# Performance work log

Measured on AMD Instinct MI355X. Metric: run time of the kernel, lower is better.

## Reference

```python
import jax, jax.numpy as jnp
import numpy as np
from functools import partial

G, N, E = 512, 256, 1024
F_IN, EMB, H, NCLS = 30, 256, 3, 2
NEG_SLOPE = 0.2
K1 = int(np.ceil(0.8 * N))   # 205
K2 = int(np.ceil(0.8 * K1))  # 164
K3 = int(np.ceil(0.8 * K2))  # 132


def _gat(x, src, dst, emask, W, asrc, adst, b):
    # Single-graph GATConv (PyG semantics, eval mode): x [n,f], edges [e] + validity mask.
    # Adds self-loops (PyG default), edge-softmax grouped by destination node.
    n = x.shape[0]
    h = (x @ W.T).reshape(n, H, EMB)                      # [n,H,C]
    a_s = (h * asrc).sum(-1)                              # [n,H]
    a_d = (h * adst).sum(-1)                              # [n,H]
    loops = jnp.arange(n, dtype=src.dtype)
    s = jnp.concatenate([src, loops])
    d = jnp.concatenate([dst, loops])
    m = jnp.concatenate([emask, jnp.ones((n,), bool)])
    logit = jax.nn.leaky_relu(a_s[s] + a_d[d], NEG_SLOPE)  # [e+n,H]
    logit = jnp.where(m[:, None], logit, -1e9)
    mx = jax.ops.segment_max(logit, d, num_segments=n)     # stable softmax per dst
    w = jnp.exp(logit - mx[d]) * m[:, None]
    den = jax.ops.segment_sum(w, d, num_segments=n)
    alpha = w / den[d]
    out = jax.ops.segment_sum(alpha[:, :, None] * h[s], d, num_segments=n)  # [n,H,C]
    return out.reshape(n, H * EMB) + b


def _pool(x, src, dst, emask, p, k):
    # TopKPooling: score = tanh((x.p)/||p||); keep top-k nodes, scale by score,
    # remap edge indices and invalidate edges touching dropped nodes.
    n = x.shape[0]
    score = jnp.tanh((x @ p) / jnp.linalg.norm(p))
    vals, perm = jax.lax.top_k(score, k)
    xn = x[perm] * vals[:, None]
    inv = jnp.full((n,), -1, jnp.int32).at[perm].set(jnp.arange(k, dtype=jnp.int32))
    ns, nd = inv[src], inv[dst]
    nm = emask & (ns >= 0) & (nd >= 0)
    return xn, jnp.maximum(ns, 0), jnp.maximum(nd, 0), nm


_gat_b = jax.vmap(_gat, in_axes=(0, 0, 0, 0, None, None, None, None))


def _pool_b(x, src, dst, m, p, k):
    return jax.vmap(partial(_pool, k=k), in_axes=(0, 0, 0, 0, None))(x, src, dst, m, p)


def _readout(x):
    # global_max_pool || global_mean_pool per graph: [G,n,d] -> [G,2d]
    return jnp.concatenate([x.max(axis=1), x.mean(axis=1)], axis=-1)


def _forward(x, edge_src, edge_dst, params):
    (W1, as1, ad1, b1, ht1w, ht1b, p1,
     W2, as2, ad2, b2, ht2w, ht2b, p2,
     W3, as3, ad3, b3, ht3w, ht3b, p3,
     l1w, l1b, l2w, l2b) = params
    src, dst = edge_src, edge_dst
    m = jnp.ones(src.shape, bool)
    h = _gat_b(x, src, dst, m, W1, as1, ad1, b1) @ ht1w.T + ht1b
    h, src, dst, m = _pool_b(h, src, dst, m, p1, K1)
    x1 = _readout(h)
    h = _gat_b(h, src, dst, m, W2, as2, ad2, b2) @ ht2w.T + ht2b
    h, src, dst, m = _pool_b(h, src, dst, m, p2, K2)
    x2 = _readout(h)
    h = _gat_b(h, src, dst, m, W3, as3, ad3, b3) @ ht3w.T + ht3b
    h, src, dst, m = _pool_b(h, src, dst, m, p3, K3)
    x3 = _readout(h)
    z = x1 + x2 + x3
    z = jax.nn.relu(z @ l1w.T + l1b)  # F.dropout is a no-op in eval mode
    return z @ l2w.T + l2b


def setup_inputs() -> dict:
    key = jax.random.key(0)
    keys = iter(jax.random.split(key, 64))
    def nrm(shape, s=0.05):
        return jax.random.normal(next(keys), shape, jnp.float32) * s
    inp = {
        "x": jax.random.normal(next(keys), (G, N, F_IN), jnp.float32),
        "edge_src": jax.random.randint(next(keys), (G, E), 0, N, jnp.int32),
        "edge_dst": jax.random.randint(next(keys), (G, E), 0, N, jnp.int32),
    }
    for i, fin in ((1, F_IN), (2, EMB), (3, EMB)):
        inp[f"W{i}"] = nrm((H * EMB, fin))
        inp[f"asrc{i}"] = nrm((H, EMB))
        inp[f"adst{i}"] = nrm((H, EMB))
        inp[f"b{i}"] = jnp.zeros((H * EMB,), jnp.float32)
        inp[f"ht{i}_w"] = nrm((EMB, H * EMB))
        inp[f"ht{i}_b"] = jnp.zeros((EMB,), jnp.float32)
        inp[f"p{i}"] = nrm((EMB,), 1.0)
    inp["lin1_w"] = nrm((EMB, 2 * EMB))
    inp["lin1_b"] = jnp.zeros((EMB,), jnp.float32)
    inp["lin2_w"] = nrm((NCLS, EMB))
    inp["lin2_b"] = jnp.zeros((NCLS,), jnp.float32)
    return inp


def reference(x, edge_src, edge_dst,
              W1, asrc1, adst1, b1, ht1_w, ht1_b, p1,
              W2, asrc2, adst2, b2, ht2_w, ht2_b, p2,
              W3, asrc3, adst3, b3, ht3_w, ht3_b, p3,
              lin1_w, lin1_b, lin2_w, lin2_b):
    params = (W1, asrc1, adst1, b1, ht1_w, ht1_b, p1,
              W2, asrc2, adst2, b2, ht2_w, ht2_b, p2,
              W3, asrc3, adst3, b3, ht3_w, ht3_b, p3,
              lin1_w, lin1_b, lin2_w, lin2_b)
    return _forward(x, edge_src, edge_dst, params)
```

## Files before the change

kernel.cpp:

```cpp
#include <hip/hip_runtime.h>
#include <hip/hip_bf16.h>

#define GG 512
#define NMAX 256
#define EE 1024
#define HH 3
#define EMB 256
#define NEDGE 1280
#define NEG 0.2f

typedef __attribute__((ext_vector_type(8))) short bf16x8;
typedef __attribute__((ext_vector_type(4))) float f32x4;
#define MFMA16(A,B,C) __builtin_amdgcn_mfma_f32_16x16x32_bf16((A),(B),(C),0,0,0)

__device__ inline void bsplit(float v, unsigned short& s0, unsigned short& s1,
                              unsigned short& s2) {
  __hip_bfloat16 b0 = __float2bfloat16(v);
  float r1 = v - __bfloat162float(b0);
  __hip_bfloat16 b1 = __float2bfloat16(r1);
  float r2 = r1 - __bfloat162float(b1);
  __hip_bfloat16 b2 = __float2bfloat16(r2);
  s0 = *(unsigned short*)&b0; s1 = *(unsigned short*)&b1; s2 = *(unsigned short*)&b2;
}

__global__ void k_prep_wa(const float* __restrict__ W, const float* __restrict__ asrc,
                          const float* __restrict__ adst, float* __restrict__ wa_s,
                          float* __restrict__ wa_d, int f) {
  int t = blockIdx.x * blockDim.x + threadIdx.x;
  int tot = HH * f;
  if (t >= 2 * tot) return;
  int which = t / tot;
  int r = t - which * tot;
  int hd = r / f, ff = r - hd * f;
  const float* a = which ? adst : asrc;
  float s = 0.f;
  for (int c = 0; c < EMB; ++c)
    s += a[hd * EMB + c] * W[(size_t)(hd * EMB + c) * f + ff];
  (which ? wa_d : wa_s)[r] = s;
}

__global__ void k_prep_mcatP(const float* __restrict__ W, const float* __restrict__ htw,
                             float* __restrict__ mcat, int f, int KP) {
  int t = blockIdx.x * blockDim.x + threadIdx.x;
  if (t >= KP * EMB) return;
  int row = t >> 8, j = t & 255;
  float s = 0.f;
  if (row < 3 * f) {
    int hd = row / f, ff = row - hd * f;
    for (int c = 0; c < EMB; ++c)
      s += htw[(size_t)j * (HH * EMB) + hd * EMB + c] * W[(size_t)(hd * EMB + c) * f + ff];
  }
  mcat[(size_t)row * EMB + j] = s;
}

__global__ void k_prep_bt3(const float* __restrict__ mcat, unsigned short* __restrict__ B0,
                           unsigned short* __restrict__ B1, unsigned short* __restrict__ B2,
                           int KP) {
  int t = blockIdx.x * blockDim.x + threadIdx.x;
  if (t >= 256 * KP) return;
  int n = t / KP, k = t - n * KP;
  float v = mcat[(size_t)k * 256 + n];
  unsigned short s0, s1, s2;
  bsplit(v, s0, s1, s2);
  B0[t] = s0; B1[t] = s1; B2[t] = s2;
}

__global__ void k_prep_bb(const float* __restrict__ b, const float* __restrict__ htw,
                          const float* __restrict__ htb, float* __restrict__ bb) {
  int j = threadIdx.x;
  float s = htb[j];
  for (int k = 0; k < HH * EMB; ++k) s += b[k] * htw[(size_t)j * (HH * EMB) + k];
  bb[j] = s;
}

__global__ void k_prep_q(const float* __restrict__ mcat, const float* __restrict__ p,
                         double* __restrict__ qv, int f) {
  int r = blockIdx.x * blockDim.x + threadIdx.x;
  if (r >= 3 * f) return;
  double s = 0.0;
  for (int c = 0; c < EMB; ++c) s += (double)mcat[(size_t)r * EMB + c] * (double)p[c];
  qv[r] = s;
}

__global__ void k_prep_sc(const float* __restrict__ p, const float* __restrict__ bb,
                          double* __restrict__ sc2) {
  __shared__ double sh[256], sh2[256];
  int t = threadIdx.x;
  double pv = (double)p[t];
  sh[t] = pv * pv;
  sh2[t] = (double)bb[t] * pv;
  __syncthreads();
  for (int s = 128; s > 0; s >>= 1) {
    if (t < s) { sh[t] += sh[t + s]; sh2[t] += sh2[t + s]; }
    __syncthreads();
  }
  if (t == 0) { sc2[0] = sh2[0]; sc2[1] = sqrt(sh[0]); }
}

__global__ __launch_bounds__(256) void k_graph(
    const int* __restrict__ src_in, const int* __restrict__ dst_in, int first,
    int* __restrict__ es, int* __restrict__ ed, int* __restrict__ em,
    const float* __restrict__ xin, const float* __restrict__ wa_s,
    const float* __restrict__ wa_d, const double* __restrict__ qv,
    const double* __restrict__ sc2,
    float4* __restrict__ a4, int* __restrict__ coff, int* __restrict__ elist,
    int* __restrict__ sel, float* __restrict__ val, int n_in, int f, int kout) {
  __shared__ float lgs[NEDGE * 3];
  __shared__ unsigned short sdst[NEDGE], ssrc[NEDGE];
  __shared__ unsigned char sval[NEDGE];
  __shared__ float sas[256][3], sad[256][3];
  __shared__ double stdt[256][3];
  __shared__ int cnt2[256];
  __shared__ int off[257];
  __shared__ int elist_s[NEDGE];
  __shared__ float sscore[256];
  __shared__ unsigned long long keys[256];
  __shared__ int inv[256];
  int g = blockIdx.x, tid = threadIdx.x;
  int etot = EE + n_in;
  cnt2[tid] = 0;
  if (tid < n_in) {
    const float* xr = xin + ((size_t)g * n_in + tid) * f;
    float s0 = 0, s1 = 0, s2 = 0, d0 = 0, d1 = 0, d2 = 0;
    double t0 = 0, t1 = 0, t2 = 0;
    for (int c = 0; c < f; ++c) {
      float xv = xr[c];
      s0 += xv * wa_s[c]; s1 += xv * wa_s[f + c]; s2 += xv * wa_s[2 * f + c];
      d0 += xv * wa_d[c]; d1 += xv * wa_d[f + c]; d2 += xv * wa_d[2 * f + c];
      double xd = (double)xv;
      t0 += xd * qv[c]; t1 += xd * qv[f + c]; t2 += xd * qv[2 * f + c];
    }
    sas[tid][0] = s0; sas[tid][1] = s1; sas[tid][2] = s2;
    sad[tid][0] = d0; sad[tid][1] = d1; sad[tid][2] = d2;
    stdt[tid][0] = t0; stdt[tid][1] = t1; stdt[tid][2] = t2;
  }
  __syncthreads();
  for (int e = tid; e < etot; e += 256) {
    int s, d, v;
    if (e < EE) {
      if (first) { s = src_in[g * EE + e]; d = dst_in[g * EE + e]; v = 1; }
      else { s = es[g * EE + e]; d = ed[g * EE + e]; v = em[g * EE + e]; }
    } else { s = d = e - EE; v = 1; }
    sdst[e] = (unsigned short)d; ssrc[e] = (unsigned short)s; sval[e] = (unsigned char)v;
    if (v) {
#pragma unroll
      for (int h = 0; h < HH; ++h) {
        float lv = sas[s][h] + sad[d][h];
        lgs[e * 3 + h] = lv > 0.f ? lv : NEG * lv;
      }
      atomicAdd(&cnt2[d], 1);
    }
  }
  __syncthreads();
  if (tid == 0) {
    int run = 0;
    for (int i = 0; i < n_in; ++i) { int c = cnt2[i]; off[i] = run; run += c; }
    off[n_in] = run;
  }
  __syncthreads();
  for (int i = tid; i <= n_in; i += 256) coff[g * 257 + i] = off[i];
  cnt2[tid] = 0;
  __syncthreads();
  for (int e = tid; e < etot; e += 256) {
    if (sval[e]) {
      int d = sdst[e];
      int pos = atomicAdd(&cnt2[d], 1);
      elist_s[off[d] + pos] = e;
    }
  }
  __syncthreads();
  if (tid < n_in) {
    int o0 = off[tid], o1 = off[tid + 1];
    for (int i = o0 + 1; i < o1; ++i) {
      int key = elist_s[i];
      int j = i - 1;
      while (j >= o0 && elist_s[j] > key) { elist_s[j + 1] = elist_s[j]; --j; }
      elist_s[j + 1] = key;
    }
    for (int q = o0; q < o1; ++q) elist[g * NEDGE + q] = elist_s[q];
  }
  __syncthreads();
  float sc = -3e38f;
  if (tid < n_in) {
    int o0 = off[tid], o1 = off[tid + 1];
    float m0 = -1e30f, m1 = -1e30f, m2 = -1e30f;
    for (int q = o0; q < o1; ++q) {
      int e = elist_s[q];
      m0 = fmaxf(m0, lgs[e * 3 + 0]);
      m1 = fmaxf(m1, lgs[e * 3 + 1]);
      m2 = fmaxf(m2, lgs[e * 3 + 2]);
    }
    float d0 = 0, d1 = 0, d2 = 0;
    for (int q = o0; q < o1; ++q) {
      int e = elist_s[q];
      d0 += expf(lgs[e * 3 + 0] - m0);
      d1 += expf(lgs[e * 3 + 1] - m1);
      d2 += expf(lgs[e * 3 + 2] - m2);
    }
    float r0 = 1.f / d0, r1 = 1.f / d1, r2 = 1.f / d2;
    double s = 0.0;
    for (int q = o0; q < o1; ++q) {
      int e = elist_s[q];
      float w0 = expf(lgs[e * 3 + 0] - m0) * r0;
      float w1 = expf(lgs[e * 3 + 1] - m1) * r1;
      float w2 = expf(lgs[e * 3 + 2] - m2) * r2;
      int src = ssrc[e];
      float4 av; av.x = w0; av.y = w1; av.z = w2; av.w = __int_as_float(src);
      a4[(size_t)g * NEDGE + e] = av;
      s += (double)w0 * stdt[src][0] + (double)w1 * stdt[src][1] + (double)w2 * stdt[src][2];
    }
    sc = (float)tanh((s + sc2[0]) / sc2[1]);
  }
  sscore[tid] = sc;
  unsigned int u = __float_as_uint(sc);
  unsigned int ord = (u & 0x80000000u) ? ~u : (u | 0x80000000u);
  unsigned long long key = ((unsigned long long)(~ord) << 32) | (unsigned int)tid;
  if (tid >= n_in) key = 0xFFFFFFFF00000000ull | (unsigned int)tid;
  keys[tid] = key;
  __syncthreads();
  for (int kk = 2; kk <= 256; kk <<= 1) {
    for (int j = kk >> 1; j > 0; j >>= 1) {
      int ixj = tid ^ j;
      if (ixj > tid) {
        unsigned long long a = keys[tid], b = keys[ixj];
        bool up = ((tid & kk) == 0);
        if (up ? (a > b) : (a < b)) { keys[tid] = b; keys[ixj] = a; }
      }
      __syncthreads();
    }
  }
  inv[tid] = -1;
  __syncthreads();
  if (tid < kout) {
    int pi = (int)(keys[tid] & 0xFFFFu);
    inv[pi] = tid;
    sel[g * 256 + tid] = pi;
    val[g * 256 + tid] = sscore[pi];
  }
  __syncthreads();
  for (int e = tid; e < EE; e += 256) {
    int s = ssrc[e], d = sdst[e], m = sval[e];
    int ns = inv[s], nd = inv[d];
    int nm = (m && ns >= 0 && nd >= 0) ? 1 : 0;
    es[g * EE + e] = ns < 0 ? 0 : ns;
    ed[g * EE + e] = nd < 0 ? 0 : nd;
    em[g * EE + e] = nm;
  }
}

template<bool F256>
__global__ __launch_bounds__(256) void k_gather_sel(
    const float* __restrict__ xin, const float4* __restrict__ a4,
    const int* __restrict__ coff, const int* __restrict__ elist,
    const int* __restrict__ sel,
    unsigned short* __restrict__ A0, unsigned short* __restrict__ A1,
    unsigned short* __restrict__ A2,
    int gc, int n_in, int n_out, int f, int KP) {
  int wid = (blockIdx.x * blockDim.x + threadIdx.x) >> 6;
  int lane = threadIdx.x & 63;
  if (wid >= gc * n_out) return;
  int g = wid / n_out, j = wid - g * n_out;
  int pi = sel[(g << 8) + j];
  int o0 = coff[g * 257 + pi], o1 = coff[g * 257 + pi + 1];
  const float* xg = xin + (size_t)g * n_in * f;
  size_t rb = ((size_t)g * n_out + j) * (size_t)KP;
  if (F256) {
    float4 acc0 = make_float4(0, 0, 0, 0);
    float4 acc1 = make_float4(0, 0, 0, 0);
    float4 acc2 = make_float4(0, 0, 0, 0);
    for (int t = o0; t < o1; ++t) {
      int e = elist[g * NEDGE + t];
      float4 a = a4[(size_t)g * NEDGE + e];
      int src = __float_as_int(a.w);
      float4 xv = ((const float4*)(xg + (size_t)src * 256))[lane];
      acc0.x += a.x * xv.x; acc0.y += a.x * xv.y; acc0.z += a.x * xv.z; acc0.w += a.x * xv.w;
      acc1.x += a.y * xv.x; acc1.y += a.y * xv.y; acc1.z += a.y * xv.z; acc1.w += a.y * xv.w;
      acc2.x += a.z * xv.x; acc2.y += a.z * xv.y; acc2.z += a.z * xv.z; acc2.w += a.z * xv.w;
    }
    float4 accs[3] = {acc0, acc1, acc2};
#pragma unroll
    for (int h = 0; h < 3; ++h) {
      size_t idx = rb + (size_t)h * 256 + lane * 4;
      ushort4 u0, u1, u2;
      bsplit(accs[h].x, u0.x, u1.x, u2.x);
      bsplit(accs[h].y, u0.y, u1.y, u2.y);
      bsplit(accs[h].z, u0.z, u1.z, u2.z);
      bsplit(accs[h].w, u0.w, u1.w, u2.w);
      *(ushort4*)&A0[idx] = u0;
      *(ushort4*)&A1[idx] = u1;
      *(ushort4*)&A2[idx] = u2;
    }
  } else {
    for (int kk = lane; kk < 96; kk += 64) {
      float v = 0.f;
      if (kk < 90) {
        int h = kk / 30, cc = kk - h * 30;
        for (int t = o0; t < o1; ++t) {
          int e = elist[g * NEDGE + t];
          float4 a = a4[(size_t)g * NEDGE + e];
          int src = __float_as_int(a.w);
          float al = (h == 0) ? a.x : ((h == 1) ? a.y : a.z);
          v += al * xg[(size_t)src * 30 + cc];
        }
      }
      unsigned short s0, s1, s2;
      bsplit(v, s0, s1, s2);
      A0[rb + kk] = s0; A1[rb + kk] = s1; A2[rb + kk] = s2;
    }
  }
}

__global__ __launch_bounds__(256, 3) void k_mgemm(
    const unsigned short* __restrict__ A0, const unsigned short* __restrict__ A1,
    const unsigned short* __restrict__ A2,
    const unsigned short* __restrict__ B0, const unsigned short* __restrict__ B1,
    const unsigned short* __restrict__ B2,
    const float* __restrict__ bias, const float* __restrict__ val,
    float* __restrict__ xout, int Mrows, int KP, int n_out, int nbx) {
  __shared__ unsigned short As[3][64 * 32];
  __shared__ unsigned short Bs[3][128 * 32];
  int tid = threadIdx.x;
  int jj = blockIdx.x & 15;
  int rr0 = (blockIdx.x >> 4) * 8 + (jj & 7);
  int cc0 = (jj >> 3) & 1;
  if (rr0 >= nbx) return;
  int row0 = rr0 * 64;
  int col0 = cc0 * 128;
  int lane = tid & 63, w = tid >> 6;
  int kg = lane >> 4, r16 = lane & 15;
  int wr = (w >> 1) * 32, wc = (w & 1) * 64;
  int sr = tid >> 2, sj = tid & 3;
  int spA = sj ^ ((sr >> 1) & 3);
  const unsigned short* Ap[3] = {A0, A1, A2};
  const unsigned short* Bp[3] = {B0, B1, B2};

  f32x4 acc[2][4];
#pragma unroll
  for (int i = 0; i < 2; ++i)
#pragma unroll
    for (int j = 0; j < 4; ++j) acc[i][j] = (f32x4){0.f, 0.f, 0.f, 0.f};

  int nkt = KP >> 5;
  for (int kt = 0; kt < nkt; ++kt) {
    int k0 = kt << 5;
    {
      int gra = row0 + sr;
#pragma unroll
      for (int p = 0; p < 3; ++p) {
        uint4 va = make_uint4(0, 0, 0, 0);
        if (gra < Mrows) va = *(const uint4*)&Ap[p][(size_t)gra * KP + k0 + (sj << 3)];
        *(uint4*)&As[p][sr * 32 + (spA << 3)] = va;
      }
    }
#pragma unroll
    for (int s = 0; s < 2; ++s) {
      int c = tid + (s << 8);
      int col = c >> 2, cg = c & 3;
      int sp = cg ^ ((col >> 1) & 3);
#pragma unroll
      for (int p = 0; p < 3; ++p) {
        uint4 vb = *(const uint4*)&Bp[p][(size_t)(col0 + col) * KP + k0 + (cg << 3)];
        *(uint4*)&Bs[p][col * 32 + (sp << 3)] = vb;
      }
    }
    __syncthreads();
    bf16x8 af[2][3], bf[4][3];
#pragma unroll
    for (int fm = 0; fm < 2; ++fm) {
      int row = wr + (fm << 4) + r16;
      int pk = kg ^ ((row >> 1) & 3);
#pragma unroll
      for (int p = 0; p < 3; ++p)
        af[fm][p] = *(const bf16x8*)&As[p][row * 32 + (pk << 3)];
    }
#pragma unroll
    for (int fn = 0; fn < 4; ++fn) {
      int col = wc + (fn << 4) + r16;
      int pk = kg ^ ((col >> 1) & 3);
#pragma unroll
      for (int p = 0; p < 3; ++p)
        bf[fn][p] = *(const bf16x8*)&Bs[p][col * 32 + (pk << 3)];
    }
#pragma unroll
    for (int fn = 0; fn < 4; ++fn)
#pragma unroll
      for (int fm = 0; fm < 2; ++fm) {
        f32x4 c = acc[fm][fn];
        c = MFMA16(af[fm][0], bf[fn][0], c);
        c = MFMA16(af[fm][0], bf[fn][1], c);
        c = MFMA16(af[fm][1], bf[fn][0], c);
        c = MFMA16(af[fm][0], bf[fn][2], c);
        c = MFMA16(af[fm][2], bf[fn][0], c);
        c = MFMA16(af[fm][1], bf[fn][1], c);
        acc[fm][fn] = c;
      }
    __syncthreads();
  }
#pragma unroll
  for (int fm = 0; fm < 2; ++fm)
#pragma unroll
    for (int fn = 0; fn < 4; ++fn) {
      int colg = col0 + wc + (fn << 4) + r16;
      float bi = bias[colg];
#pragma unroll
      for (int rr = 0; rr < 4; ++rr) {
        int rowg = row0 + wr + (fm << 4) + (kg << 2) + rr;
        if (rowg < Mrows) {
          int gg = rowg / n_out, j = rowg - gg * n_out;
          xout[((size_t)gg * n_out + j) * EMB + colg] =
              (acc[fm][fn][rr] + bi) * val[(gg << 8) + j];
        }
      }
    }
}

__global__ void k_readout(const float* __restrict__ x, float* __restrict__ z,
                          int n_out, int g0) {
  int g = blockIdx.x, c = threadIdx.x;
  float mx = -3e38f, sm = 0.f;
  for (int j = 0; j < n_out; ++j) {
    float v = x[((size_t)g * n_out + j) * EMB + c];
    mx = fmaxf(mx, v);
    sm += v;
  }
  z[(size_t)(g0 + g) * 512 + c] += mx;
  z[(size_t)(g0 + g) * 512 + 256 + c] += sm / (float)n_out;
}

__global__ void k_mlp(const float* __restrict__ z, const float* __restrict__ l1w,
                      const float* __restrict__ l1b, const float* __restrict__ l2w,
                      const float* __restrict__ l2b, float* __restrict__ out) {
  __shared__ float zs[512];
  __shared__ float h1[256];
  int g = blockIdx.x, tid = threadIdx.x;
  zs[tid] = z[(size_t)g * 512 + tid];
  zs[256 + tid] = z[(size_t)g * 512 + 256 + tid];
  __syncthreads();
  float s = l1b[tid];
  for (int c = 0; c < 512; ++c) s += zs[c] * l1w[(size_t)tid * 512 + c];
  h1[tid] = s > 0.f ? s : 0.f;
  __syncthreads();
  if (tid < 2) {
    float o = l2b[tid];
    for (int c = 0; c < 256; ++c) o += h1[c] * l2w[(size_t)tid * 256 + c];
    out[g * 2 + tid] = o;
  }
}

extern "C" void kernel_launch(void* const* d_in, const int* in_sizes, int n_in_cnt,
                              void* d_out, int out_size, void* d_ws, size_t ws_size,
                              hipStream_t stream) {
  (void)in_sizes; (void)n_in_cnt; (void)out_size;
  const float* x0 = (const float*)d_in[0];
  const int* e_src = (const int*)d_in[1];
  const int* e_dst = (const int*)d_in[2];
  struct LP { const float *W, *as, *ad, *b, *hw, *hb, *p; int f, nin, nout, KP; };
  LP L[3];
  for (int l = 0; l < 3; ++l) {
    int base = 3 + l * 7;
    L[l].W  = (const float*)d_in[base + 0];
    L[l].as = (const float*)d_in[base + 1];
    L[l].ad = (const float*)d_in[base + 2];
    L[l].b  = (const float*)d_in[base + 3];
    L[l].hw = (const float*)d_in[base + 4];
    L[l].hb = (const float*)d_in[base + 5];
    L[l].p  = (const float*)d_in[base + 6];
  }
  L[0].f = 30;  L[1].f = 256; L[2].f = 256;
  L[0].nin = 256; L[0].nout = 205; L[0].KP = 96;
  L[1].nin = 205; L[1].nout = 164; L[1].KP = 768;
  L[2].nin = 164; L[2].nout = 132; L[2].KP = 768;
  const float* l1w = (const float*)d_in[24];
  const float* l1b = (const float*)d_in[25];
  const float* l2w = (const float*)d_in[26];
  const float* l2b = (const float*)d_in[27];
  float* out = (float*)d_out;

  char* w = (char*)d_ws;
  char* wend = w + ws_size;
  auto alloc = [&](size_t bytes) {
    char* r = w; w += (bytes + 255) & ~(size_t)255; return r;
  };
  float*  z = (float*)alloc((size_t)GG * 512 * 4);
  float *wa_s[3], *wa_d[3], *mcatP[3], *bbv[3];
  unsigned short *bt0[3], *bt1[3], *bt2[3];
  double *qv[3], *sc2[3];
  for (int l = 0; l < 3; ++l) {
    int KP = (l == 0) ? 96 : 768;
    wa_s[l]  = (float*)alloc((size_t)HH * 256 * 4);
    wa_d[l]  = (float*)alloc((size_t)HH * 256 * 4);
    mcatP[l] = (float*)alloc((size_t)768 * EMB * 4);
    bbv[l]   = (float*)alloc((size_t)EMB * 4);
    bt0[l]   = (unsigned short*)alloc((size_t)256 * KP * 2);
    bt1[l]   = (unsigned short*)alloc((size_t)256 * KP * 2);
    bt2[l]   = (unsigned short*)alloc((size_t)256 * KP * 2);
    qv[l]    = (double*)alloc((size_t)768 * 8);
    sc2[l]   = (double*)alloc(256);
  }

  const size_t AMAX = (size_t)164 * 768;
  const size_t APAD = (size_t)64 * 768;
  size_t fixed_used = (size_t)(w - (char*)d_ws);
  size_t per_g = (size_t)205 * EMB * 4
               + AMAX * 2 * 3
               + (size_t)NEDGE * 16
               + (size_t)EE * 4 * 3
               + (size_t)257 * 4 + (size_t)NEDGE * 4
               + (size_t)256 * 4 * 2
               + 24 * 256;
  size_t avail = (ws_size > fixed_used + 1048576) ? (ws_size - fixed_used - 1048576) : 0;
  int Gc = (int)(avail / per_g);
  if (Gc > GG) Gc = GG;
  if (Gc < 1) Gc = 1;
  int nchunks = (GG + Gc - 1) / Gc;
  Gc = (GG + nchunks - 1) / nchunks;

  float*  xbuf = (float*)alloc((size_t)Gc * 205 * EMB * 4);
  unsigned short* AP0 = (unsigned short*)alloc(((size_t)Gc * AMAX + APAD) * 2);
  unsigned short* AP1 = (unsigned short*)alloc(((size_t)Gc * AMAX + APAD) * 2);
  unsigned short* AP2 = (unsigned short*)alloc(((size_t)Gc * AMAX + APAD) * 2);
  float4* a4   = (float4*)alloc((size_t)Gc * NEDGE * 16);
  int*    es   = (int*)alloc((size_t)Gc * EE * 4);
  int*    ed   = (int*)alloc((size_t)Gc * EE * 4);
  int*    em   = (int*)alloc((size_t)Gc * EE * 4);
  int*    coff = (int*)alloc((size_t)Gc * 257 * 4);
  int*    elist= (int*)alloc((size_t)Gc * NEDGE * 4);
  int*    sel  = (int*)alloc((size_t)Gc * 256 * 4);
  float*  val  = (float*)alloc((size_t)Gc * 256 * 4);
  if (w > wend) return;

  (void)hipMemsetAsync(z, 0, (size_t)GG * 512 * 4, stream);

  for (int l = 0; l < 3; ++l) {
    int f = L[l].f, KP = L[l].KP;
    k_prep_wa<<<(2 * HH * f + 255) / 256, 256, 0, stream>>>(L[l].W, L[l].as, L[l].ad, wa_s[l], wa_d[l], f);
    k_prep_mcatP<<<(KP * EMB + 255) / 256, 256, 0, stream>>>(L[l].W, L[l].hw, mcatP[l], f, KP);
    k_prep_bt3<<<(256 * KP + 255) / 256, 256, 0, stream>>>(mcatP[l], bt0[l], bt1[l], bt2[l], KP);
    k_prep_bb<<<1, 256, 0, stream>>>(L[l].b, L[l].hw, L[l].hb, bbv[l]);
    k_prep_q<<<(3 * f + 255) / 256, 256, 0, stream>>>(mcatP[l], L[l].p, qv[l], f);
    k_prep_sc<<<1, 256, 0, stream>>>(L[l].p, bbv[l], sc2[l]);
  }

  for (int g0 = 0; g0 < GG; g0 += Gc) {
    int gc = (GG - g0 < Gc) ? (GG - g0) : Gc;
    const float* xin = x0 + (size_t)g0 * 256 * 30;
    for (int l = 0; l < 3; ++l) {
      int f = L[l].f, nin = L[l].nin, nout = L[l].nout, KP = L[l].KP;
      k_graph<<<gc, 256, 0, stream>>>(e_src + (size_t)g0 * EE, e_dst + (size_t)g0 * EE,
                                      (l == 0) ? 1 : 0, es, ed, em,
                                      xin, wa_s[l], wa_d[l], qv[l], sc2[l],
                                      a4, coff, elist, sel, val, nin, f, nout);
      { int waves = gc * nout;
        if (f == 256)
          k_gather_sel<true><<<(waves * 64 + 255) / 256, 256, 0, stream>>>(
              xin, a4, coff, elist, sel, AP0, AP1, AP2, gc, nin, nout, f, KP);
        else
          k_gather_sel<false><<<(waves * 64 + 255) / 256, 256, 0, stream>>>(
              xin, a4, coff, elist, sel, AP0, AP1, AP2, gc, nin, nout, f, KP);
      }
      { int Mrows = gc * nout;
        int nbx = (Mrows + 63) / 64;
        int nblk = ((nbx + 7) / 8) * 16;
        k_mgemm<<<nblk, 256, 0, stream>>>(AP0, AP1, AP2, bt0[l], bt1[l], bt2[l],
                                          bbv[l], val, xbuf, Mrows, KP, nout, nbx);
      }
      k_readout<<<gc, 256, 0, stream>>>(xbuf, z, nout, g0);
      xin = xbuf;
    }
  }
  k_mlp<<<GG, 256, 0, stream>>>(z, l1w, l1b, l2w, l2b, out);
}
```

Before: 1.827 ms.

## Retile split-bf16 GEMM to 128x64 with 512 threads; parallel prefix scan

The MFMA GEMM moves from 64x128 tiles on 256 threads to 128x64 tiles on 512 threads (8 waves, each computing a 32x32 sub-tile), and the block index mapping is reworked to match. Smaller per-wave accumulators lower register pressure, and the larger row tile changes how A and B tiles are reused. Separately, k_graph's serial single-thread offset scan is replaced by a Hillis-Steele parallel scan over 256 entries, trading a serial loop for log-step barriers. Padding and workspace reserve grow to cover the larger row tile.

```diff
diff --git a/kernel.cpp b/kernel.cpp
--- a/kernel.cpp
+++ b/kernel.cpp
@@ -111,6 +111,7 @@
   __shared__ float sas[256][3], sad[256][3];
   __shared__ double stdt[256][3];
   __shared__ int cnt2[256];
+  __shared__ int scn[256];
   __shared__ int off[257];
   __shared__ int elist_s[NEDGE];
   __shared__ float sscore[256];
@@ -152,11 +153,16 @@
     }
   }
   __syncthreads();
-  if (tid == 0) {
-    int run = 0;
-    for (int i = 0; i < n_in; ++i) { int c = cnt2[i]; off[i] = run; run += c; }
-    off[n_in] = run;
-  }
+  scn[tid] = cnt2[tid];
+  __syncthreads();
+  for (int d = 1; d < 256; d <<= 1) {
+    int t = (tid >= d) ? scn[tid - d] : 0;
+    __syncthreads();
+    scn[tid] += t;
+    __syncthreads();
+  }
+  off[tid + 1] = scn[tid];
+  if (tid == 0) off[0] = 0;
   __syncthreads();
   for (int i = tid; i <= n_in; i += 256) coff[g * 257 + i] = off[i];
   cnt2[tid] = 0;
@@ -310,61 +316,60 @@
   }
 }
 
-__global__ __launch_bounds__(256, 3) void k_mgemm(
+__global__ __launch_bounds__(512, 2) void k_mgemm(
     const unsigned short* __restrict__ A0, const unsigned short* __restrict__ A1,
     const unsigned short* __restrict__ A2,
     const unsigned short* __restrict__ B0, const unsigned short* __restrict__ B1,
     const unsigned short* __restrict__ B2,
     const float* __restrict__ bias, const float* __restrict__ val,
     float* __restrict__ xout, int Mrows, int KP, int n_out, int nbx) {
-  __shared__ unsigned short As[3][64 * 32];
-  __shared__ unsigned short Bs[3][128 * 32];
+  __shared__ unsigned short As[3][128 * 32];
+  __shared__ unsigned short Bs[3][64 * 32];
   int tid = threadIdx.x;
-  int jj = blockIdx.x & 15;
-  int rr0 = (blockIdx.x >> 4) * 8 + (jj & 7);
-  int cc0 = (jj >> 3) & 1;
+  int jj = blockIdx.x & 31;
+  int rr0 = (blockIdx.x >> 5) * 8 + (jj & 7);
+  int cc0 = jj >> 3;
   if (rr0 >= nbx) return;
-  int row0 = rr0 * 64;
-  int col0 = cc0 * 128;
+  int row0 = rr0 * 128;
+  int col0 = cc0 * 64;
   int lane = tid & 63, w = tid >> 6;
   int kg = lane >> 4, r16 = lane & 15;
-  int wr = (w >> 1) * 32, wc = (w & 1) * 64;
-  int sr = tid >> 2, sj = tid & 3;
-  int spA = sj ^ ((sr >> 1) & 3);
+  int wr = (w >> 1) * 32, wc = (w & 1) * 32;
+  int sra = tid >> 2, sja = tid & 3;
+  int spa = sja ^ ((sra >> 1) & 3);
+  int srb = (tid & 255) >> 2, sjb = tid & 3;
+  int spb = sjb ^ ((srb >> 1) & 3);
   const unsigned short* Ap[3] = {A0, A1, A2};
   const unsigned short* Bp[3] = {B0, B1, B2};
 
-  f32x4 acc[2][4];
+  f32x4 acc[2][2];
 #pragma unroll
   for (int i = 0; i < 2; ++i)
 #pragma unroll
-    for (int j = 0; j < 4; ++j) acc[i][j] = (f32x4){0.f, 0.f, 0.f, 0.f};
+    for (int j = 0; j < 2; ++j) acc[i][j] = (f32x4){0.f, 0.f, 0.f, 0.f};
 
   int nkt = KP >> 5;
   for (int kt = 0; kt < nkt; ++kt) {
     int k0 = kt << 5;
     {
-      int gra = row0 + sr;
+      int gra = row0 + sra;
 #pragma unroll
       for (int p = 0; p < 3; ++p) {
         uint4 va = make_uint4(0, 0, 0, 0);
-        if (gra < Mrows) va = *(const uint4*)&Ap[p][(size_t)gra * KP + k0 + (sj << 3)];
-        *(uint4*)&As[p][sr * 32 + (spA << 3)] = va;
-      }
-    }
-#pragma unroll
-    for (int s = 0; s < 2; ++s) {
-      int c = tid + (s << 8);
-      int col = c >> 2, cg = c & 3;
-      int sp = cg ^ ((col >> 1) & 3);
+        if (gra < Mrows) va = *(const uint4*)&Ap[p][(size_t)gra * KP + k0 + (sja << 3)];
+        *(uint4*)&As[p][sra * 32 + (spa << 3)] = va;
+      }
+    }
+    if (tid < 256) {
+      int grb = col0 + srb;
 #pragma unroll
       for (int p = 0; p < 3; ++p) {
-        uint4 vb = *(const uint4*)&Bp[p][(size_t)(col0 + col) * KP + k0 + (cg << 3)];
-        *(uint4*)&Bs[p][col * 32 + (sp << 3)] = vb;
+        uint4 vb = *(const uint4*)&Bp[p][(size_t)grb * KP + k0 + (sjb << 3)];
+        *(uint4*)&Bs[p][srb * 32 + (spb << 3)] = vb;
       }
     }
     __syncthreads();
-    bf16x8 af[2][3], bf[4][3];
+    bf16x8 af[2][3], bf[2][3];
 #pragma unroll
     for (int fm = 0; fm < 2; ++fm) {
       int row = wr + (fm << 4) + r16;
@@ -374,7 +379,7 @@
         af[fm][p] = *(const bf16x8*)&As[p][row * 32 + (pk << 3)];
     }
 #pragma unroll
-    for (int fn = 0; fn < 4; ++fn) {
+    for (int fn = 0; fn < 2; ++fn) {
       int col = wc + (fn << 4) + r16;
       int pk = kg ^ ((col >> 1) & 3);
 #pragma unroll
@@ -382,9 +387,9 @@
         bf[fn][p] = *(const bf16x8*)&Bs[p][col * 32 + (pk << 3)];
     }
 #pragma unroll
-    for (int fn = 0; fn < 4; ++fn)
-#pragma unroll
-      for (int fm = 0; fm < 2; ++fm) {
+    for (int fm = 0; fm < 2; ++fm)
+#pragma unroll
+      for (int fn = 0; fn < 2; ++fn) {
         f32x4 c = acc[fm][fn];
         c = MFMA16(af[fm][0], bf[fn][0], c);
         c = MFMA16(af[fm][0], bf[fn][1], c);
@@ -399,7 +404,7 @@
 #pragma unroll
   for (int fm = 0; fm < 2; ++fm)
 #pragma unroll
-    for (int fn = 0; fn < 4; ++fn) {
+    for (int fn = 0; fn < 2; ++fn) {
       int colg = col0 + wc + (fn << 4) + r16;
       float bi = bias[colg];
 #pragma unroll
@@ -499,7 +504,7 @@
   }
 
   const size_t AMAX = (size_t)164 * 768;
-  const size_t APAD = (size_t)64 * 768;
+  const size_t APAD = (size_t)128 * 768;
   size_t fixed_used = (size_t)(w - (char*)d_ws);
   size_t per_g = (size_t)205 * EMB * 4
                + AMAX * 2 * 3
@@ -508,7 +513,7 @@
                + (size_t)257 * 4 + (size_t)NEDGE * 4
                + (size_t)256 * 4 * 2
                + 24 * 256;
-  size_t avail = (ws_size > fixed_used + 1048576) ? (ws_size - fixed_used - 1048576) : 0;
+  size_t avail = (ws_size > fixed_used + 2097152) ? (ws_size - fixed_used - 2097152) : 0;
   int Gc = (int)(avail / per_g);
   if (Gc > GG) Gc = GG;
   if (Gc < 1) Gc = 1;
@@ -559,9 +564,9 @@
               xin, a4, coff, elist, sel, AP0, AP1, AP2, gc, nin, nout, f, KP);
       }
       { int Mrows = gc * nout;
-        int nbx = (Mrows + 63) / 64;
-        int nblk = ((nbx + 7) / 8) * 16;
-        k_mgemm<<<nblk, 256, 0, stream>>>(AP0, AP1, AP2, bt0[l], bt1[l], bt2[l],
+        int nbx = (Mrows + 127) / 128;
+        int nblk = ((nbx + 7) / 8) * 32;
+        k_mgemm<<<nblk, 512, 0, stream>>>(AP0, AP1, AP2, bt0[l], bt1[l], bt2[l],
                                           bbv[l], val, xbuf, Mrows, KP, nout, nbx);
       }
       k_readout<<<gc, 256, 0, stream>>>(xbuf, z, nout, g0);
```

Measured after the change: 1.880 ms. 2.9% more time.
